# Optimization experiments

Measured on AMD Instinct MI355X. Metric: run time of the kernel, lower is better.

The kernel has to match this reference:

```python
import jax, jax.numpy as jnp
import numpy as np

# tiny-cuda-nn HashGrid config from the module
N_LEVELS = 12
F_PER_LEVEL = 2
LOG2_T = 16
T = 1 << LOG2_T            # 65536 entries per level
BASE_RES = 4
PER_LEVEL_SCALE = 1.61
HASH_PRIME_Y = np.uint32(2654435761)
HIDDEN = 256
OUT = 3
N_POINTS = 1048576

# per-level scale / resolution (tcnn: scale = base*s^l - 1, res = ceil(scale)+1)
_LEVEL_SCALES = [BASE_RES * (PER_LEVEL_SCALE ** l) - 1.0 for l in range(N_LEVELS)]
_LEVEL_RES = [int(np.ceil(s)) + 1 for s in _LEVEL_SCALES]

_CORNERS = np.array([[0, 0], [1, 0], [0, 1], [1, 1]], dtype=np.uint32)  # [4,2]


def hash_encode(x, tables):
    """x: [N,2] in [0,1); tables: [L,T,F]. Returns [N, L*F]."""
    offs_u = jnp.asarray(_CORNERS)                      # [4,2] uint32
    offs_f = offs_u.astype(x.dtype)                     # [4,2]
    feats = []
    for l in range(N_LEVELS):
        s = _LEVEL_SCALES[l]
        res = _LEVEL_RES[l]
        pos = x * jnp.asarray(s, x.dtype) + 0.5         # [N,2]
        p0f = jnp.floor(pos)
        w = pos - p0f                                   # [N,2] frac, differentiable
        p0 = p0f.astype(jnp.uint32)                     # [N,2]
        c = p0[:, None, :] + offs_u[None]               # [N,4,2] corner coords
        # bilinear weight per corner: prod over dims of (w if offset==1 else 1-w)
        wc = jnp.where(offs_f[None] == 1.0, w[:, None, :], 1.0 - w[:, None, :]).prod(-1)  # [N,4]
        if res * res <= T:
            # dense (tight grid) indexing
            cx = jnp.minimum(c[..., 0], np.uint32(res - 1))
            cy = jnp.minimum(c[..., 1], np.uint32(res - 1))
            idx = cx + cy * np.uint32(res)
        else:
            # spatial hash: x*1 XOR y*prime, masked to table size
            idx = (c[..., 0] ^ (c[..., 1] * HASH_PRIME_Y)) & np.uint32(T - 1)
        f = tables[l][idx.astype(jnp.int32)]            # [N,4,F] gather
        feats.append((wc[..., None] * f).sum(axis=1))   # [N,F]
    return jnp.concatenate(feats, axis=-1)              # [N, L*F]


def setup_inputs() -> dict:
    key = jax.random.key(0)
    ks = jax.random.split(key, 10)
    x = jax.random.uniform(ks[0], (N_POINTS, 2), dtype=jnp.float32)
    # tcnn initializes hash tables uniform in [-1e-4, 1e-4]
    tables = jax.random.uniform(ks[1], (N_LEVELS, T, F_PER_LEVEL), dtype=jnp.float32,
                                minval=-1e-4, maxval=1e-4)
    d_in = N_LEVELS * F_PER_LEVEL

    def lin(k, fan_in, fan_out):
        bound = 1.0 / np.sqrt(fan_in)
        kw, kb = jax.random.split(k)
        W = jax.random.uniform(kw, (fan_in, fan_out), dtype=jnp.float32, minval=-bound, maxval=bound)
        b = jax.random.uniform(kb, (fan_out,), dtype=jnp.float32, minval=-bound, maxval=bound)
        return W, b

    W1, b1 = lin(ks[2], d_in, HIDDEN)
    W2, b2 = lin(ks[3], HIDDEN, HIDDEN)
    W3, b3 = lin(ks[4], HIDDEN, HIDDEN)
    Wo, bo = lin(ks[5], HIDDEN, OUT)
    return {"x": x, "tables": tables, "W1": W1, "b1": b1, "W2": W2, "b2": b2,
            "W3": W3, "b3": b3, "Wo": Wo, "bo": bo}


def reference(x, tables, W1, b1, W2, b2, W3, b3, Wo, bo):
    enc = hash_encode(x, tables)                        # [N,24]
    h = jax.nn.relu(enc @ W1 + b1)
    h = jax.nn.relu(h @ W2 + b2)
    h = jax.nn.relu(h @ W3 + b3)
    return h @ Wo + bo                                  # [N,3]
```

## Files before the change

### kernel.cpp

```cpp
#include <hip/hip_runtime.h>

typedef _Float16 f16;
typedef _Float16 f16x2 __attribute__((ext_vector_type(2)));
typedef _Float16 f16x4 __attribute__((ext_vector_type(4)));
typedef _Float16 f16x8 __attribute__((ext_vector_type(8)));
typedef float    f32x4 __attribute__((ext_vector_type(4)));

#define ES 40
#define NPTS 128


static __device__ const float c_scale[12] = {
  3.0f, 5.44f, 9.3684f, 15.693124f, 25.87592964f, 42.2702467204f,
  68.665097219844f, 111.16080652394884f, 179.5788985035576f,
  289.7320265907278f, 467.0785628110717f, 752.6064861258255f };
static __device__ const unsigned c_res[12] = {4,7,11,17,27,44,70,113,181,291,469,754};

__global__ __launch_bounds__(256) void prep_weights(
    const float* __restrict__ W1, const float* __restrict__ W2,
    const float* __restrict__ W3, const float* __restrict__ Wo,
    f16* __restrict__ ws)
{
  int i = blockIdx.x * 256 + threadIdx.x;
  if (i < 8192) {
    int o = i >> 5, k = i & 31;
    ws[i] = (k < 24) ? (f16)W1[k * 256 + o] : (f16)0.0f;
  } else if (i < 73728) {
    int j = i - 8192; int o = j >> 8, k = j & 255;
    ws[i] = (f16)W2[k * 256 + o];
  } else if (i < 139264) {
    int j = i - 73728; int o = j >> 8, k = j & 255;
    ws[i] = (f16)W3[k * 256 + o];
  } else if (i < 143360) {
    int j = i - 139264; int o = j >> 8, k = j & 255;
    ws[i] = (o < 3) ? (f16)Wo[k * 3 + o] : (f16)0.0f;
  }
}

template<bool NEXT_OUT>
__device__ __forceinline__ void layer256_pipe(
    f16* __restrict__ h, const f16* __restrict__ WT,
    const f32x4* bv, f16x8* cur0, f16x8* cur1,
    const f16* __restrict__ WTn, const float* __restrict__ bn,
    f16x8* nxt0, f16x8* nxt1, f32x4* bvn, f16x8* aout,
    const int* vbase, const int* wbase, int w, int l15, int g)
{
  f32x4 acc[4][8];
  #pragma unroll
  for (int mt = 0; mt < 4; ++mt)
    #pragma unroll
    for (int nt = 0; nt < 8; ++nt) acc[mt][nt] = bv[mt];

  f16x8 abuf[3][4];
  #pragma unroll
  for (int mt = 0; mt < 4; ++mt) { abuf[0][mt] = cur0[mt]; abuf[1][mt] = cur1[mt]; }

  const char* hb = (const char*)h;
  #pragma unroll
  for (int ks = 0; ks < 8; ++ks) {
    if (ks < 6) {
      #pragma unroll
      for (int mt = 0; mt < 4; ++mt)
        abuf[(ks+2)%3][mt] = *(const f16x8*)(WT + (w*64 + mt*16 + l15)*256 + (ks+2)*32 + g*8);
    } else if (ks == 6) {
      if (NEXT_OUT) {
        #pragma unroll
        for (int q = 0; q < 4; ++q)
          aout[q] = *(const f16x8*)(WTn + l15*256 + q*32 + g*8);
      } else {
        #pragma unroll
        for (int mt = 0; mt < 4; ++mt)
          nxt0[mt] = *(const f16x8*)(WTn + (w*64 + mt*16 + l15)*256 + g*8);
        #pragma unroll
        for (int mt = 0; mt < 4; ++mt)
          bvn[mt] = *(const f32x4*)(bn + w*64 + mt*16 + g*4);
      }
    } else {
      if (NEXT_OUT) {
        #pragma unroll
        for (int q = 0; q < 4; ++q)
          aout[4+q] = *(const f16x8*)(WTn + l15*256 + (4+q)*32 + g*8);
      } else {
        #pragma unroll
        for (int mt = 0; mt < 4; ++mt)
          nxt1[mt] = *(const f16x8*)(WTn + (w*64 + mt*16 + l15)*256 + 32 + g*8);
      }
    }
    #pragma unroll
    for (int nt = 0; nt < 8; ++nt) {
      f16x8 b = *(const f16x8*)(hb + vbase[ks] + nt*8192);
      #pragma unroll
      for (int mt = 0; mt < 4; ++mt)
        acc[mt][nt] = __builtin_amdgcn_mfma_f32_16x16x32_f16(abuf[ks%3][mt], b, acc[mt][nt], 0, 0, 0);
    }
  }
  __syncthreads();
  #pragma unroll
  for (int mt = 0; mt < 4; ++mt) {
    #pragma unroll
    for (int nt = 0; nt < 8; ++nt) {
      f16x4 hv;
      #pragma unroll
      for (int r = 0; r < 4; ++r)
        hv[r] = (f16)fmaxf(acc[mt][nt][r], 0.0f);
      *(f16x4*)((char*)h + wbase[mt] + nt*8192) = hv;
    }
  }
  __syncthreads();
}

__global__ __launch_bounds__(256, 2) void hashmlp_kernel(
    const float* __restrict__ x, const float* __restrict__ tables,
    const float* __restrict__ b1, const float* __restrict__ b2,
    const float* __restrict__ b3, const float* __restrict__ bo,
    const f16* __restrict__ ws, float* __restrict__ out)
{
  __shared__ __align__(16) f16 s_enc[NPTS * ES];
  __shared__ __align__(16) f16 s_h[NPTS * 256];

  const int tid = threadIdx.x;
  const int blk = blockIdx.x;
  const int w = tid >> 6, lane = tid & 63;
  const int l15 = lane & 15, g = lane >> 4;

  const f16* W1T = ws;
  const f16* W2T = ws + 8192;
  const f16* W3T = ws + 73728;
  const f16* WoT = ws + 139264;

  f16x8 a1[4], pn0[4], pn1[4];
  f32x4 bvA[4], bvB[4];
  #pragma unroll
  for (int mt = 0; mt < 4; ++mt) {
    a1[mt]  = *(const f16x8*)(W1T + (w*64 + mt*16 + l15)*32 + g*8);
    pn0[mt] = *(const f16x8*)(W2T + (w*64 + mt*16 + l15)*256 + g*8);
    pn1[mt] = *(const f16x8*)(W2T + (w*64 + mt*16 + l15)*256 + 32 + g*8);
    bvA[mt] = *(const f32x4*)(b1 + w*64 + mt*16 + g*4);
    bvB[mt] = *(const f32x4*)(b2 + w*64 + mt*16 + g*4);
  }
  float bo0 = bo[0], bo1 = bo[1], bo2 = bo[2];

  int vbase[8], wbase[4];
  {
    int K = (l15 & 7) << 4;
    #pragma unroll
    for (int ks = 0; ks < 8; ++ks)
      vbase[ks] = l15*512 + ((ks*64 + g*16) ^ K);
    #pragma unroll
    for (int mt = 0; mt < 4; ++mt)
      wbase[mt] = l15*512 + (((w*64 + mt*16 + g*4)*2) ^ K);
  }

  {
    int p = tid >> 1, sub = tid & 1;
    int gp = blk * NPTS + p;
    float2 xy = ((const float2*)x)[gp];
    #pragma unroll
    for (int j = 0; j < 6; ++j) {
      int l = sub * 6 + j;
      float s = c_scale[l];
      unsigned res = c_res[l];
      float px = __fadd_rn(__fmul_rn(xy.x, s), 0.5f);
      float py = __fadd_rn(__fmul_rn(xy.y, s), 0.5f);
      float fx = floorf(px), fy = floorf(py);
      float wx = px - fx, wy = py - fy;
      unsigned ix = (unsigned)fx, iy = (unsigned)fy;
      unsigned i00, i10, i01, i11;
      if (res * res <= 65536u) {
        unsigned rm = res - 1u;
        unsigned x0 = min(ix, rm), x1 = min(ix + 1u, rm);
        unsigned y0 = min(iy, rm), y1 = min(iy + 1u, rm);
        i00 = x0 + y0 * res; i10 = x1 + y0 * res;
        i01 = x0 + y1 * res; i11 = x1 + y1 * res;
      } else {
        unsigned h0 = iy * 2654435761u, h1 = (iy + 1u) * 2654435761u;
        i00 = (ix ^ h0) & 65535u;  i10 = ((ix + 1u) ^ h0) & 65535u;
        i01 = (ix ^ h1) & 65535u;  i11 = ((ix + 1u) ^ h1) & 65535u;
      }
      const float2* tb = (const float2*)(tables + l * 131072);
      float2 f00 = tb[i00], f10 = tb[i10], f01 = tb[i01], f11 = tb[i11];
      float w00 = (1.f - wx) * (1.f - wy), w10 = wx * (1.f - wy);
      float w01 = (1.f - wx) * wy,         w11 = wx * wy;
      float e0 = w00 * f00.x + w10 * f10.x + w01 * f01.x + w11 * f11.x;
      float e1 = w00 * f00.y + w10 * f10.y + w01 * f01.y + w11 * f11.y;
      f16x2 pk; pk[0] = (f16)e0; pk[1] = (f16)e1;
      *(f16x2*)(&s_enc[p * ES + l * 2]) = pk;
    }
    f16x4 z; z[0] = (f16)0.0f; z[1] = (f16)0.0f; z[2] = (f16)0.0f; z[3] = (f16)0.0f;
    *(f16x4*)(&s_enc[p * ES + 24 + sub * 4]) = z;
  }
  __syncthreads();

  {
    f32x4 acc[4][8];
    #pragma unroll
    for (int mt = 0; mt < 4; ++mt)
      #pragma unroll
      for (int nt = 0; nt < 8; ++nt) acc[mt][nt] = bvA[mt];
    #pragma unroll
    for (int nt = 0; nt < 8; ++nt) {
      f16x8 b = *(const f16x8*)(&s_enc[(nt*16 + l15) * ES + g*8]);
      #pragma unroll
      for (int mt = 0; mt < 4; ++mt)
        acc[mt][nt] = __builtin_amdgcn_mfma_f32_16x16x32_f16(a1[mt], b, acc[mt][nt], 0, 0, 0);
    }
    #pragma unroll
    for (int mt = 0; mt < 4; ++mt) {
      #pragma unroll
      for (int nt = 0; nt < 8; ++nt) {
        f16x4 hv;
        #pragma unroll
        for (int r = 0; r < 4; ++r)
          hv[r] = (f16)fmaxf(acc[mt][nt][r], 0.0f);
        *(f16x4*)((char*)s_h + wbase[mt] + nt*8192) = hv;
      }
    }
  }
  __syncthreads();

  f16x8 qn0[4], qn1[4], aout[8];
  f32x4 bvC[4];
  layer256_pipe<false>(s_h, W2T, bvB, pn0, pn1, W3T, b3, qn0, qn1, bvC, aout,
                       vbase, wbase, w, l15, g);
  layer256_pipe<true >(s_h, W3T, bvC, qn0, qn1, WoT, nullptr, pn0, pn1, bvC, aout,
                       vbase, wbase, w, l15, g);

  {
    f32x4 acc0 = (f32x4)0.0f, acc1 = (f32x4)0.0f;
    const char* hb = (const char*)s_h;
    #pragma unroll
    for (int ks = 0; ks < 8; ++ks) {
      f16x8 b0 = *(const f16x8*)(hb + vbase[ks] + (2*w+0)*8192);
      f16x8 b1v = *(const f16x8*)(hb + vbase[ks] + (2*w+1)*8192);
      acc0 = __builtin_amdgcn_mfma_f32_16x16x32_f16(aout[ks], b0, acc0, 0, 0, 0);
      acc1 = __builtin_amdgcn_mfma_f32_16x16x32_f16(aout[ks], b1v, acc1, 0, 0, 0);
    }
    if (g == 0) {
      int gp0 = blk * NPTS + (2*w+0) * 16 + l15;
      int gp1 = blk * NPTS + (2*w+1) * 16 + l15;
      out[gp0 * 3 + 0] = acc0[0] + bo0;
      out[gp0 * 3 + 1] = acc0[1] + bo1;
      out[gp0 * 3 + 2] = acc0[2] + bo2;
      out[gp1 * 3 + 0] = acc1[0] + bo0;
      out[gp1 * 3 + 1] = acc1[1] + bo1;
      out[gp1 * 3 + 2] = acc1[2] + bo2;
    }
  }
}

extern "C" void kernel_launch(void* const* d_in, const int* in_sizes, int n_in,
                              void* d_out, int out_size, void* d_ws, size_t ws_size,
                              hipStream_t stream) {
  const float* x  = (const float*)d_in[0];
  const float* tb = (const float*)d_in[1];
  const float* W1 = (const float*)d_in[2];
  const float* b1 = (const float*)d_in[3];
  const float* W2 = (const float*)d_in[4];
  const float* b2 = (const float*)d_in[5];
  const float* W3 = (const float*)d_in[6];
  const float* b3 = (const float*)d_in[7];
  const float* Wo = (const float*)d_in[8];
  const float* bo = (const float*)d_in[9];
  f16* ws = (f16*)d_ws;

  prep_weights<<<560, 256, 0, stream>>>(W1, W2, W3, Wo, ws);
  hashmlp_kernel<<<8192, 256, 0, stream>>>(x, tb, b1, b2, b3, bo, ws, (float*)d_out);
}
```

Baseline: 365.2 us.

## Split hash encoding into separate kernel and stream encodings into LDS via global_load_lds

Moves the hash-grid gather and interpolation into a standalone encode kernel that writes padded fp16 encodings to workspace. The MLP kernel then pulls each block's encodings into LDS with direct global-to-LDS loads, issued alongside the weight register loads. The aim is to stop latency-bound table gathers from stalling the MFMA-heavy MLP blocks, which run at low occupancy. The cost is an extra round trip of about 80 MB to global memory and one more launch. A fallback to the fused kernel is kept for when the workspace is too small.

```diff
diff --git a/kernel.cpp b/kernel.cpp
--- a/kernel.cpp
+++ b/kernel.cpp
@@ -9,12 +9,52 @@
 #define ES 40
 #define NPTS 128
 
+#define ENC_OFF 143360
+#define WS_NEED (2ull*ENC_OFF + 2ull*1048576ull*40ull)
+
+#define GLOAD_LDS16(g, l) __builtin_amdgcn_global_load_lds( \
+    (const __attribute__((address_space(1))) void*)(g), \
+    (__attribute__((address_space(3))) void*)(l), 16, 0, 0)
+
+__device__ __forceinline__ f16* hswz(f16* base, int p, int fbyte) {
+  return (f16*)((char*)base + p * 512 + (fbyte ^ ((p & 7) << 4)));
+}
 
 static __device__ const float c_scale[12] = {
   3.0f, 5.44f, 9.3684f, 15.693124f, 25.87592964f, 42.2702467204f,
   68.665097219844f, 111.16080652394884f, 179.5788985035576f,
   289.7320265907278f, 467.0785628110717f, 752.6064861258255f };
 static __device__ const unsigned c_res[12] = {4,7,11,17,27,44,70,113,181,291,469,754};
+
+__device__ __forceinline__ f16x2 enc_level(float2 xy, int l, const float* __restrict__ tables) {
+  float s = c_scale[l];
+  unsigned res = c_res[l];
+  float px = __fadd_rn(__fmul_rn(xy.x, s), 0.5f);
+  float py = __fadd_rn(__fmul_rn(xy.y, s), 0.5f);
+  float fx = floorf(px), fy = floorf(py);
+  float wx = px - fx, wy = py - fy;
+  unsigned ix = (unsigned)fx, iy = (unsigned)fy;
+  unsigned i00, i10, i01, i11;
+  if (res * res <= 65536u) {
+    unsigned rm = res - 1u;
+    unsigned x0 = min(ix, rm), x1 = min(ix + 1u, rm);
+    unsigned y0 = min(iy, rm), y1 = min(iy + 1u, rm);
+    i00 = x0 + y0 * res; i10 = x1 + y0 * res;
+    i01 = x0 + y1 * res; i11 = x1 + y1 * res;
+  } else {
+    unsigned h0 = iy * 2654435761u, h1 = (iy + 1u) * 2654435761u;
+    i00 = (ix ^ h0) & 65535u;  i10 = ((ix + 1u) ^ h0) & 65535u;
+    i01 = (ix ^ h1) & 65535u;  i11 = ((ix + 1u) ^ h1) & 65535u;
+  }
+  const float2* tb = (const float2*)(tables + l * 131072);
+  float2 f00 = tb[i00], f10 = tb[i10], f01 = tb[i01], f11 = tb[i11];
+  float w00 = (1.f - wx) * (1.f - wy), w10 = wx * (1.f - wy);
+  float w01 = (1.f - wx) * wy,         w11 = wx * wy;
+  float e0 = w00 * f00.x + w10 * f10.x + w01 * f01.x + w11 * f11.x;
+  float e1 = w00 * f00.y + w10 * f10.y + w01 * f01.y + w11 * f11.y;
+  f16x2 pk; pk[0] = (f16)e0; pk[1] = (f16)e1;
+  return pk;
+}
 
 __global__ __launch_bounds__(256) void prep_weights(
     const float* __restrict__ W1, const float* __restrict__ W2,
@@ -37,6 +77,29 @@
   }
 }
 
+__global__ __launch_bounds__(256) void encode_kernel(
+    const float* __restrict__ x, const float* __restrict__ tables,
+    f16* __restrict__ encp)
+{
+  int gp = blockIdx.x * 256 + threadIdx.x;
+  float2 xy = ((const float2*)x)[gp];
+  f16x8 c[5];
+  #pragma unroll
+  for (int ch = 0; ch < 5; ++ch)
+    #pragma unroll
+    for (int j = 0; j < 8; ++j) c[ch][j] = (f16)0.0f;
+  #pragma unroll
+  for (int l = 0; l < 12; ++l) {
+    f16x2 e = enc_level(xy, l, tables);
+    c[l >> 2][(l & 3) * 2 + 0] = e[0];
+    c[l >> 2][(l & 3) * 2 + 1] = e[1];
+  }
+  f16* row = encp + (size_t)gp * ES;
+  #pragma unroll
+  for (int ch = 0; ch < 5; ++ch)
+    *(f16x8*)(row + ch * 8) = c[ch];
+}
+
 template<bool NEXT_OUT>
 __device__ __forceinline__ void layer256_pipe(
     f16* __restrict__ h, const f16* __restrict__ WT,
@@ -109,87 +172,16 @@
   __syncthreads();
 }
 
-__global__ __launch_bounds__(256, 2) void hashmlp_kernel(
-    const float* __restrict__ x, const float* __restrict__ tables,
-    const float* __restrict__ b1, const float* __restrict__ b2,
-    const float* __restrict__ b3, const float* __restrict__ bo,
-    const f16* __restrict__ ws, float* __restrict__ out)
-{
-  __shared__ __align__(16) f16 s_enc[NPTS * ES];
-  __shared__ __align__(16) f16 s_h[NPTS * 256];
-
-  const int tid = threadIdx.x;
-  const int blk = blockIdx.x;
-  const int w = tid >> 6, lane = tid & 63;
-  const int l15 = lane & 15, g = lane >> 4;
-
-  const f16* W1T = ws;
-  const f16* W2T = ws + 8192;
+__device__ __forceinline__ void mlp_body(
+    f16* s_enc, f16* s_h, const f16* ws,
+    const float* b1, const float* b2, const float* b3, const float* bo,
+    float* out, int blk, int w, int l15, int g,
+    f16x8* a1, f16x8* pn0, f16x8* pn1, f32x4* bvA, f32x4* bvB,
+    const int* vbase, const int* wbase)
+{
   const f16* W3T = ws + 73728;
   const f16* WoT = ws + 139264;
-
-  f16x8 a1[4], pn0[4], pn1[4];
-  f32x4 bvA[4], bvB[4];
-  #pragma unroll
-  for (int mt = 0; mt < 4; ++mt) {
-    a1[mt]  = *(const f16x8*)(W1T + (w*64 + mt*16 + l15)*32 + g*8);
-    pn0[mt] = *(const f16x8*)(W2T + (w*64 + mt*16 + l15)*256 + g*8);
-    pn1[mt] = *(const f16x8*)(W2T + (w*64 + mt*16 + l15)*256 + 32 + g*8);
-    bvA[mt] = *(const f32x4*)(b1 + w*64 + mt*16 + g*4);
-    bvB[mt] = *(const f32x4*)(b2 + w*64 + mt*16 + g*4);
-  }
   float bo0 = bo[0], bo1 = bo[1], bo2 = bo[2];
-
-  int vbase[8], wbase[4];
-  {
-    int K = (l15 & 7) << 4;
-    #pragma unroll
-    for (int ks = 0; ks < 8; ++ks)
-      vbase[ks] = l15*512 + ((ks*64 + g*16) ^ K);
-    #pragma unroll
-    for (int mt = 0; mt < 4; ++mt)
-      wbase[mt] = l15*512 + (((w*64 + mt*16 + g*4)*2) ^ K);
-  }
-
-  {
-    int p = tid >> 1, sub = tid & 1;
-    int gp = blk * NPTS + p;
-    float2 xy = ((const float2*)x)[gp];
-    #pragma unroll
-    for (int j = 0; j < 6; ++j) {
-      int l = sub * 6 + j;
-      float s = c_scale[l];
-      unsigned res = c_res[l];
-      float px = __fadd_rn(__fmul_rn(xy.x, s), 0.5f);
-      float py = __fadd_rn(__fmul_rn(xy.y, s), 0.5f);
-      float fx = floorf(px), fy = floorf(py);
-      float wx = px - fx, wy = py - fy;
-      unsigned ix = (unsigned)fx, iy = (unsigned)fy;
-      unsigned i00, i10, i01, i11;
-      if (res * res <= 65536u) {
-        unsigned rm = res - 1u;
-        unsigned x0 = min(ix, rm), x1 = min(ix + 1u, rm);
-        unsigned y0 = min(iy, rm), y1 = min(iy + 1u, rm);
-        i00 = x0 + y0 * res; i10 = x1 + y0 * res;
-        i01 = x0 + y1 * res; i11 = x1 + y1 * res;
-      } else {
-        unsigned h0 = iy * 2654435761u, h1 = (iy + 1u) * 2654435761u;
-        i00 = (ix ^ h0) & 65535u;  i10 = ((ix + 1u) ^ h0) & 65535u;
-        i01 = (ix ^ h1) & 65535u;  i11 = ((ix + 1u) ^ h1) & 65535u;
-      }
-      const float2* tb = (const float2*)(tables + l * 131072);
-      float2 f00 = tb[i00], f10 = tb[i10], f01 = tb[i01], f11 = tb[i11];
-      float w00 = (1.f - wx) * (1.f - wy), w10 = wx * (1.f - wy);
-      float w01 = (1.f - wx) * wy,         w11 = wx * wy;
-      float e0 = w00 * f00.x + w10 * f10.x + w01 * f01.x + w11 * f11.x;
-      float e1 = w00 * f00.y + w10 * f10.y + w01 * f01.y + w11 * f11.y;
-      f16x2 pk; pk[0] = (f16)e0; pk[1] = (f16)e1;
-      *(f16x2*)(&s_enc[p * ES + l * 2]) = pk;
-    }
-    f16x4 z; z[0] = (f16)0.0f; z[1] = (f16)0.0f; z[2] = (f16)0.0f; z[3] = (f16)0.0f;
-    *(f16x4*)(&s_enc[p * ES + 24 + sub * 4]) = z;
-  }
-  __syncthreads();
 
   {
     f32x4 acc[4][8];
@@ -220,6 +212,7 @@
 
   f16x8 qn0[4], qn1[4], aout[8];
   f32x4 bvC[4];
+  const f16* W2T = ws + 8192;
   layer256_pipe<false>(s_h, W2T, bvB, pn0, pn1, W3T, b3, qn0, qn1, bvC, aout,
                        vbase, wbase, w, l15, g);
   layer256_pipe<true >(s_h, W3T, bvC, qn0, qn1, WoT, nullptr, pn0, pn1, bvC, aout,
@@ -246,6 +239,118 @@
       out[gp1 * 3 + 2] = acc1[2] + bo2;
     }
   }
+}
+
+__global__ __launch_bounds__(256, 2) void hashmlp_main(
+    const f16* __restrict__ encp,
+    const float* __restrict__ b1, const float* __restrict__ b2,
+    const float* __restrict__ b3, const float* __restrict__ bo,
+    const f16* __restrict__ ws, float* __restrict__ out)
+{
+  __shared__ __align__(16) f16 s_enc[NPTS * ES];
+  __shared__ __align__(16) f16 s_h[NPTS * 256];
+
+  const int tid = threadIdx.x;
+  const int blk = blockIdx.x;
+  const int w = tid >> 6, lane = tid & 63;
+  const int l15 = lane & 15, g = lane >> 4;
+
+  {
+    const char* gsrc = (const char*)(encp) + (size_t)blk * (NPTS * ES * 2);
+    char* lb = (char*)s_enc;
+    GLOAD_LDS16(gsrc + (0*256 + w*64 + lane)*16, lb + (0*256 + w*64)*16);
+    GLOAD_LDS16(gsrc + (1*256 + w*64 + lane)*16, lb + (1*256 + w*64)*16);
+    if (w < 2)
+      GLOAD_LDS16(gsrc + (512 + w*64 + lane)*16, lb + (512 + w*64)*16);
+  }
+
+  const f16* W1T = ws;
+  const f16* W2T = ws + 8192;
+
+  f16x8 a1[4], pn0[4], pn1[4];
+  f32x4 bvA[4], bvB[4];
+  #pragma unroll
+  for (int mt = 0; mt < 4; ++mt) {
+    a1[mt]  = *(const f16x8*)(W1T + (w*64 + mt*16 + l15)*32 + g*8);
+    pn0[mt] = *(const f16x8*)(W2T + (w*64 + mt*16 + l15)*256 + g*8);
+    pn1[mt] = *(const f16x8*)(W2T + (w*64 + mt*16 + l15)*256 + 32 + g*8);
+    bvA[mt] = *(const f32x4*)(b1 + w*64 + mt*16 + g*4);
+    bvB[mt] = *(const f32x4*)(b2 + w*64 + mt*16 + g*4);
+  }
+
+  int vbase[8], wbase[4];
+  {
+    int K = (l15 & 7) << 4;
+    #pragma unroll
+    for (int ks = 0; ks < 8; ++ks)
+      vbase[ks] = l15*512 + ((ks*64 + g*16) ^ K);
+    #pragma unroll
+    for (int mt = 0; mt < 4; ++mt)
+      wbase[mt] = l15*512 + (((w*64 + mt*16 + g*4)*2) ^ K);
+  }
+
+  __syncthreads();
+
+  mlp_body(s_enc, s_h, ws, b1, b2, b3, bo, out, blk, w, l15, g,
+           a1, pn0, pn1, bvA, bvB, vbase, wbase);
+}
+
+__global__ __launch_bounds__(256, 2) void hashmlp_mono(
+    const float* __restrict__ x, const float* __restrict__ tables,
+    const float* __restrict__ b1, const float* __restrict__ b2,
+    const float* __restrict__ b3, const float* __restrict__ bo,
+    const f16* __restrict__ ws, float* __restrict__ out)
+{
+  __shared__ __align__(16) f16 s_enc[NPTS * ES];
+  __shared__ __align__(16) f16 s_h[NPTS * 256];
+
+  const int tid = threadIdx.x;
+  const int blk = blockIdx.x;
+  const int w = tid >> 6, lane = tid & 63;
+  const int l15 = lane & 15, g = lane >> 4;
+
+  const f16* W1T = ws;
+  const f16* W2T = ws + 8192;
+
+  f16x8 a1[4], pn0[4], pn1[4];
+  f32x4 bvA[4], bvB[4];
+  #pragma unroll
+  for (int mt = 0; mt < 4; ++mt) {
+    a1[mt]  = *(const f16x8*)(W1T + (w*64 + mt*16 + l15)*32 + g*8);
+    pn0[mt] = *(const f16x8*)(W2T + (w*64 + mt*16 + l15)*256 + g*8);
+    pn1[mt] = *(const f16x8*)(W2T + (w*64 + mt*16 + l15)*256 + 32 + g*8);
+    bvA[mt] = *(const f32x4*)(b1 + w*64 + mt*16 + g*4);
+    bvB[mt] = *(const f32x4*)(b2 + w*64 + mt*16 + g*4);
+  }
+
+  int vbase[8], wbase[4];
+  {
+    int K = (l15 & 7) << 4;
+    #pragma unroll
+    for (int ks = 0; ks < 8; ++ks)
+      vbase[ks] = l15*512 + ((ks*64 + g*16) ^ K);
+    #pragma unroll
+    for (int mt = 0; mt < 4; ++mt)
+      wbase[mt] = l15*512 + (((w*64 + mt*16 + g*4)*2) ^ K);
+  }
+
+  {
+    int p = tid >> 1, sub = tid & 1;
+    int gp = blk * NPTS + p;
+    float2 xy = ((const float2*)x)[gp];
+    #pragma unroll
+    for (int j = 0; j < 6; ++j) {
+      int l = sub * 6 + j;
+      f16x2 pk = enc_level(xy, l, tables);
+      *(f16x2*)(&s_enc[p * ES + l * 2]) = pk;
+    }
+    f16x4 z; z[0] = (f16)0.0f; z[1] = (f16)0.0f; z[2] = (f16)0.0f; z[3] = (f16)0.0f;
+    *(f16x4*)(&s_enc[p * ES + 24 + sub * 4]) = z;
+  }
+  __syncthreads();
+
+  mlp_body(s_enc, s_h, ws, b1, b2, b3, bo, out, blk, w, l15, g,
+           a1, pn0, pn1, bvA, bvB, vbase, wbase);
 }
 
 extern "C" void kernel_launch(void* const* d_in, const int* in_sizes, int n_in,
@@ -264,5 +369,11 @@
   f16* ws = (f16*)d_ws;
 
   prep_weights<<<560, 256, 0, stream>>>(W1, W2, W3, Wo, ws);
-  hashmlp_kernel<<<8192, 256, 0, stream>>>(x, tb, b1, b2, b3, bo, ws, (float*)d_out);
-}
+  if (ws_size >= WS_NEED) {
+    f16* encp = ws + ENC_OFF;
+    encode_kernel<<<4096, 256, 0, stream>>>(x, tb, encp);
+    hashmlp_main<<<8192, 256, 0, stream>>>(encp, b1, b2, b3, bo, ws, (float*)d_out);
+  } else {
+    hashmlp_mono<<<8192, 256, 0, stream>>>(x, tb, b1, b2, b3, bo, ws, (float*)d_out);
+  }
+}
```

New measurement: 391.0 us. 1.07x slower.
